# Optimization experiments

Hardware: AMD Instinct MI355X
Metric: run time of the kernel (lower is better)

Reference implementation:

```python
import jax, jax.numpy as jnp
import numpy as np

N, S, C, G = 50000, 16, 96, 6  # points, neighbours, embed_channels, groups
EPS = 1e-5


def bn(x, gamma, beta):
    # BatchNorm1d eval mode with default running stats (mean=0, var=1)
    return x * (gamma / jnp.sqrt(1.0 + EPS)) + beta


def setup_inputs() -> dict:
    key = jax.random.key(0)
    ks = jax.random.split(key, 16)
    d = {}
    d["feat"] = jax.random.normal(ks[0], (N, C), jnp.float32)
    d["coord"] = jax.random.uniform(ks[1], (N, 3), jnp.float32)
    d["reference_index"] = jax.random.randint(ks[2], (N, S), 0, N)

    def lin(k, fi, fo):
        return jax.random.normal(k, (fi, fo), jnp.float32) * 0.02

    # linear_q / linear_k / linear_v
    d["Wq"] = lin(ks[3], C, C); d["bq"] = jnp.zeros((C,), jnp.float32)
    d["gq"] = jnp.ones((C,), jnp.float32); d["betaq"] = jnp.zeros((C,), jnp.float32)
    d["Wk"] = lin(ks[4], C, C); d["bk"] = jnp.zeros((C,), jnp.float32)
    d["gk"] = jnp.ones((C,), jnp.float32); d["betak"] = jnp.zeros((C,), jnp.float32)
    d["Wv"] = lin(ks[5], C, C); d["bv"] = jnp.zeros((C,), jnp.float32)
    # linear_p_bias: Linear(3,C) -> BN -> ReLU -> Linear(C,C)
    d["Wp1"] = lin(ks[6], 3, C); d["bp1"] = jnp.zeros((C,), jnp.float32)
    d["gp"] = jnp.ones((C,), jnp.float32); d["betap"] = jnp.zeros((C,), jnp.float32)
    d["Wp2"] = lin(ks[7], C, C); d["bp2"] = jnp.zeros((C,), jnp.float32)
    # weight_encoding: Linear(C,G) -> BN(G) -> ReLU -> Linear(G,G)
    d["Ww1"] = lin(ks[8], C, G); d["bw1"] = jnp.zeros((G,), jnp.float32)
    d["gw"] = jnp.ones((G,), jnp.float32); d["betaw"] = jnp.zeros((G,), jnp.float32)
    d["Ww2"] = lin(ks[9], G, G); d["bw2"] = jnp.zeros((G,), jnp.float32)
    return d


def reference(feat, coord, Wq, bq, gq, betaq, Wk, bk, gk, betak, Wv, bv,
              Wp1, bp1, gp, betap, Wp2, bp2, Ww1, bw1, gw, betaw, Ww2, bw2,
              reference_index):
    q = jax.nn.relu(bn(feat @ Wq + bq, gq, betaq))          # [N, C]
    k = jax.nn.relu(bn(feat @ Wk + bk, gk, betak))          # [N, C]
    v = feat @ Wv + bv                                       # [N, C]

    # pointops.grouping: gather neighbours, with_xyz gives relative positions
    kg = k[reference_index]                                  # [N, S, C]
    vg = v[reference_index]                                  # [N, S, C]
    pos = coord[reference_index] - coord[:, None, :]         # [N, S, 3]

    relation_qk = kg - q[:, None, :]                         # [N, S, C]
    peb = jax.nn.relu(bn(pos @ Wp1 + bp1, gp, betap)) @ Wp2 + bp2  # [N, S, C]
    relation_qk = relation_qk + peb
    vg = vg + peb

    w = jax.nn.relu(bn(relation_qk @ Ww1 + bw1, gw, betaw)) @ Ww2 + bw2  # [N, S, G]
    w = jax.nn.softmax(w, axis=1)                            # softmax over neighbours
    mask = jnp.sign(reference_index + 1).astype(w.dtype)     # [N, S]
    w = w * mask[..., None]

    vg = vg.reshape(N, S, G, C // G)                         # [N, S, G, i]
    out = jnp.einsum('nsgi,nsg->ngi', vg, w).reshape(N, C)   # [N, C]
    return out
```

## Files before the change

### kernel.cpp

```cpp
#include <hip/hip_runtime.h>

typedef unsigned short u16;
typedef __attribute__((ext_vector_type(8))) short short8;
typedef __attribute__((ext_vector_type(4))) float f32x4;

__device__ __forceinline__ u16 f2bf(float f) {
    unsigned int x = __float_as_uint(f);
    unsigned int r = x + 0x7fffu + ((x >> 16) & 1u);
    return (u16)(r >> 16);
}
__device__ __forceinline__ unsigned int pk2(float lo, float hi) {
    return ((unsigned int)f2bf(hi) << 16) | (unsigned int)f2bf(lo);
}
__device__ __forceinline__ float2 bf2x(unsigned int d) {
    float2 r;
    r.x = __uint_as_float(d << 16);
    r.y = __uint_as_float(d & 0xffff0000u);
    return r;
}
__device__ __forceinline__ void bf8x(uint4 v, float* o) {
    float2 a = bf2x(v.x); o[0] = a.x; o[1] = a.y;
    float2 b = bf2x(v.y); o[2] = b.x; o[3] = b.y;
    float2 c = bf2x(v.z); o[4] = c.x; o[5] = c.y;
    float2 d = bf2x(v.w); o[6] = d.x; o[7] = d.y;
}
__device__ __forceinline__ float rfl_f(float x) {
    return __uint_as_float(__builtin_amdgcn_readfirstlane(__float_as_uint(x)));
}

#define CC 96
#define SS 16
#define GG 6
#define BN_INV 0.99999500003749969f
#define ABLK 768
#define TOTW (ABLK * 4)

#define WB_ODD 2496
#define WB_WPW 4992
#define WB_TOT 5304

__global__ __launch_bounds__(256) void prep_kernel(
    const float* __restrict__ Wq, const float* __restrict__ Wk, const float* __restrict__ Wv,
    const float* __restrict__ Wp2, const float* __restrict__ Ww1,
    const float* __restrict__ bp2, const float* __restrict__ bw1,
    u16* __restrict__ WcatT, unsigned int* __restrict__ gWB, float* __restrict__ cvec)
{
    int t = blockIdx.x * 256 + threadIdx.x;
    if (t < 13824) {
        int c = t / 48, j2 = t % 48;
        const float* src = (c < 96) ? Wq : (c < 192) ? Wk : Wv;
        int cc = c % 96;
        float a = src[(2 * j2) * CC + cc];
        float b = src[(2 * j2 + 1) * CC + cc];
        ((unsigned int*)WcatT)[t] = pk2(a, b);
    } else if (t < 13824 + WB_TOT) {
        int i = t - 13824;
        if (i < WB_WPW) {
            int arr = i / WB_ODD;
            int r = i % WB_ODD;
            int c2 = r / 52, rr = r % 52;
            unsigned int d = 0;
            if (rr < 48) {
                int c = 2 * c2 + arr;
                d = pk2(Wp2[(2 * rr) * CC + c], Wp2[(2 * rr + 1) * CC + c]);
            }
            gWB[i] = d;
        } else {
            int r = i - WB_WPW;
            int g = r / 52, rr = r % 52;
            unsigned int d = 0;
            if (rr < 48) {
                float a = 0.f, b = 0.f;
                for (int c = 0; c < CC; ++c) {
                    float wg = Ww1[c * GG + g];
                    a = fmaf(Wp2[(2 * rr) * CC + c], wg, a);
                    b = fmaf(Wp2[(2 * rr + 1) * CC + c], wg, b);
                }
                d = pk2(a, b);
            }
            gWB[i] = d;
        }
    } else if (t < 13824 + WB_TOT + GG) {
        int g = t - (13824 + WB_TOT);
        float acc = bw1[g];
        for (int c = 0; c < CC; ++c)
            acc = fmaf(bp2[c], Ww1[c * GG + g], acc);
        cvec[g] = acc;
    }
}

__global__ __launch_bounds__(256) void fcvt_kernel(
    const float* __restrict__ feat, u16* __restrict__ featB, int total4)
{
    int i = blockIdx.x * 256 + threadIdx.x;
    if (i < total4) {
        float4 v = *(const float4*)(feat + (size_t)i * 4);
        ushort4 o;
        o.x = f2bf(v.x); o.y = f2bf(v.y); o.z = f2bf(v.z); o.w = f2bf(v.w);
        *(ushort4*)(featB + (size_t)i * 4) = o;
    }
}

#define SBS 104
__global__ __launch_bounds__(256, 2) void gemm_qkv(
    const u16* __restrict__ featB, const u16* __restrict__ WcatT,
    const float* __restrict__ bq, const float* __restrict__ gq, const float* __restrict__ betaq,
    const float* __restrict__ bk, const float* __restrict__ gk, const float* __restrict__ betak,
    const float* __restrict__ bv, const float* __restrict__ Ww1,
    u16* __restrict__ v_bf, float* __restrict__ KW1, float* __restrict__ qW1, int N)
{
    __shared__ u16 sB[288 * SBS];
    const int t = threadIdx.x;

    for (int i = t; i < 288 * 12; i += 256) {
        int row = i / 12, c8 = i % 12;
        *(float4*)(sB + row * SBS + c8 * 8) = *(const float4*)(WcatT + row * CC + c8 * 8);
    }
    __syncthreads();

    const int wave = t >> 6, lane = t & 63;
    const int m = lane & 15, quad = lane >> 4;
    const int rowbase = blockIdx.x * 64 + wave * 16;

    int arow = rowbase + m;
    if (arow >= N) arow = 0;

    short8 a[3];
    #pragma unroll
    for (int kk = 0; kk < 3; ++kk)
        a[kk] = *(const short8*)(featB + (size_t)arow * CC + kk * 32 + quad * 8);

    f32x4 acc[18];
    #pragma unroll
    for (int nt = 0; nt < 18; ++nt) acc[nt] = (f32x4){0.f, 0.f, 0.f, 0.f};

    #pragma unroll
    for (int kk = 0; kk < 3; ++kk) {
        #pragma unroll
        for (int nt = 0; nt < 18; ++nt) {
            short8 b = *(const short8*)(sB + (nt * 16 + m) * SBS + kk * 32 + quad * 8);
            acc[nt] = __builtin_amdgcn_mfma_f32_16x16x32_bf16(a[kk], b, acc[nt], 0, 0, 0);
        }
    }

    int orow[4];
    #pragma unroll
    for (int i = 0; i < 4; ++i) orow[i] = rowbase + quad * 4 + i;
    const int cloc = m;

    #pragma unroll
    for (int nt6 = 0; nt6 < 6; ++nt6) {
        int c = nt6 * 16 + cloc;
        float bvv = bv[c];
        #pragma unroll
        for (int i = 0; i < 4; ++i)
            if (orow[i] < N)
                v_bf[(size_t)orow[i] * CC + c] = f2bf(acc[12 + nt6][i] + bvv);
    }

    #pragma unroll
    for (int mat = 0; mat < 2; ++mat) {
        const float* bb_ = mat ? bk : bq;
        const float* gg_ = mat ? gk : gq;
        const float* be_ = mat ? betak : betaq;
        float red[4][6];
        #pragma unroll
        for (int i = 0; i < 4; ++i)
            #pragma unroll
            for (int g = 0; g < 6; ++g) red[i][g] = 0.f;

        #pragma unroll
        for (int nt6 = 0; nt6 < 6; ++nt6) {
            int nt = mat * 6 + nt6;
            int c = nt6 * 16 + cloc;
            float bb = bb_[c], sc = gg_[c] * BN_INV, be = be_[c];
            float w1r[6];
            #pragma unroll
            for (int g = 0; g < 6; ++g) w1r[g] = Ww1[c * GG + g];
            #pragma unroll
            for (int i = 0; i < 4; ++i) {
                float act = fmaxf(0.f, fmaf(acc[nt][i] + bb, sc, be));
                #pragma unroll
                for (int g = 0; g < 6; ++g)
                    red[i][g] = fmaf(act, w1r[g], red[i][g]);
            }
        }
        #pragma unroll
        for (int st = 1; st < 16; st <<= 1)
            #pragma unroll
            for (int i = 0; i < 4; ++i)
                #pragma unroll
                for (int g = 0; g < 6; ++g)
                    red[i][g] += __shfl_xor(red[i][g], st);

        float* dst = mat ? KW1 : qW1;
        #pragma unroll
        for (int g = 0; g < 6; ++g)
            if (cloc == g)
                #pragma unroll
                for (int i = 0; i < 4; ++i)
                    if (orow[i] < N)
                        dst[(size_t)orow[i] * 8 + g] = red[i][g];
    }
}

__global__ __launch_bounds__(256) void attn_kernel(
    const float* __restrict__ coord, const int* __restrict__ ref,
    const float* __restrict__ Wp1, const float* __restrict__ bp1, const float* __restrict__ gp, const float* __restrict__ betap,
    const float* __restrict__ bp2,
    const float* __restrict__ gw, const float* __restrict__ betaw,
    const float* __restrict__ Ww2, const float* __restrict__ bw2,
    const u16* __restrict__ v_bf, const float* __restrict__ KW1, const float* __restrict__ qW1,
    const unsigned int* __restrict__ gWB, const float* __restrict__ cvec,
    float* __restrict__ out, int N)
{
    __shared__ __align__(16) unsigned int sWB[WB_TOT];
    __shared__ __align__(16) unsigned int shh[4][832];
    __shared__ __align__(16) uint4 swt[4][SS];
    __shared__ __align__(16) float sHs[4][600];
    __shared__ __align__(16) float4 sposx[4][SS];
    __shared__ int sidxx[4][SS];

    const int t = threadIdx.x;
    for (int i = t; i < WB_TOT; i += 256) sWB[i] = gWB[i];
    __syncthreads();

    const int w = t >> 6, lane = t & 63;
    const int wid = blockIdx.x * 4 + w;
    unsigned int* shw = shh[w];
    uint4* swtw = swt[w];
    float* sHsw = sHs[w];
    float4* sposw = sposx[w];
    int* sidxw = sidxx[w];

    const int  L = (lane < 48) ? lane : 47;
    const bool actv = lane < 48;
    const int  cA = 2 * L;
    const int  gL = L >> 3;
    const int  s16 = lane & 15, qq = lane >> 4;

    const float spA = gp[cA] * BN_INV, spB = gp[cA + 1] * BN_INV;
    const float w1xA = Wp1[cA] * spA, w1yA = Wp1[CC + cA] * spA, w1zA = Wp1[2 * CC + cA] * spA;
    const float w1xB = Wp1[cA + 1] * spB, w1yB = Wp1[CC + cA + 1] * spB, w1zB = Wp1[2 * CC + cA + 1] * spB;
    const float b1A = fmaf(bp1[cA], spA, betap[cA]);
    const float b1B = fmaf(bp1[cA + 1], spB, betap[cA + 1]);
    const float bpA = bp2[cA], bpB = bp2[cA + 1];

    int idxreg = 0;
    if (lane < SS && wid < N) idxreg = ref[wid * SS + s16];

    for (int n = wid; n < N; n += TOTW) {
        if (lane < SS) sidxw[s16] = idxreg;
        float4 kAv = {0,0,0,0}; float2 kBv = {0,0};
        if (lane < SS) {
            int j = idxreg;
            float4 P;
            P.x = coord[j * 3 + 0] - coord[n * 3 + 0];
            P.y = coord[j * 3 + 1] - coord[n * 3 + 1];
            P.z = coord[j * 3 + 2] - coord[n * 3 + 2];
            P.w = 0.f;
            sposw[s16] = P;
            const float* kr = KW1 + (size_t)idxreg * 8;
            kAv = *(const float4*)kr; kBv = *(const float2*)(kr + 4);
        }
        float qc[GG];
        {
            int nu = __builtin_amdgcn_readfirstlane(n);
            const float* qr = qW1 + (size_t)nu * 8;
            #pragma unroll
            for (int g = 0; g < GG; ++g)
                qc[g] = rfl_f(cvec[g] - qr[g]);
        }
        {
            int nn = n + TOTW;
            if (lane < SS && nn < N) idxreg = ref[nn * SS + s16];
        }

        if (actv) {
            #pragma unroll
            for (int s = 0; s < SS; ++s) {
                float4 P = sposw[s];
                float hA = fmaxf(0.f, fmaf(P.x, w1xA, fmaf(P.y, w1yA, fmaf(P.z, w1zA, b1A))));
                float hB = fmaxf(0.f, fmaf(P.x, w1xB, fmaf(P.y, w1yB, fmaf(P.z, w1zB, b1B))));
                shw[s * 52 + L] = pk2(hA, hB);
            }
        }

        float acc[GG];
        {
            const unsigned int* hrow = shw + 52 * s16 + 12 * qq;
            const unsigned int* wbase = sWB + WB_WPW + 12 * qq;
            #pragma unroll
            for (int g = 0; g < GG; ++g) acc[g] = 0.f;
            #pragma unroll
            for (int c3 = 0; c3 < 3; ++c3) {
                float hg[8];
                bf8x(*(const uint4*)(hrow + 4 * c3), hg);
                #pragma unroll
                for (int g = 0; g < GG; ++g) {
                    float wg[8];
                    bf8x(*(const uint4*)(wbase + g * 52 + 4 * c3), wg);
                    float a = acc[g];
                    #pragma unroll
                    for (int u = 0; u < 8; ++u)
                        a = fmaf(hg[u], wg[u], a);
                    acc[g] = a;
                }
            }
            #pragma unroll
            for (int g = 0; g < GG; ++g) {
                acc[g] += __shfl_xor(acc[g], 16);
                acc[g] += __shfl_xor(acc[g], 32);
            }
        }

        unsigned int vpre[SS];
        #pragma unroll
        for (int s = 0; s < SS; ++s) {
            int jj = sidxw[s];
            vpre[s] = *(const unsigned int*)(v_bf + (size_t)jj * CC + cA);
        }

        if (lane < SS) {
            float tv[GG];
            tv[0] = acc[0] + kAv.x + qc[0];
            tv[1] = acc[1] + kAv.y + qc[1];
            tv[2] = acc[2] + kAv.z + qc[2];
            tv[3] = acc[3] + kAv.w + qc[3];
            tv[4] = acc[4] + kBv.x + qc[4];
            tv[5] = acc[5] + kBv.y + qc[5];
            float a6[GG];
            #pragma unroll
            for (int g = 0; g < GG; ++g)
                a6[g] = fmaxf(0.f, fmaf(tv[g], gw[g] * BN_INV, betaw[g]));
            float e[GG];
            #pragma unroll
            for (int gg2 = 0; gg2 < GG; ++gg2) {
                float lv = bw2[gg2];
                #pragma unroll
                for (int g2 = 0; g2 < GG; ++g2)
                    lv = fmaf(a6[g2], Ww2[g2 * GG + gg2], lv);
                e[gg2] = __expf(lv);
            }
            float wgt[GG];
            #pragma unroll
            for (int g = 0; g < GG; ++g) {
                float ssum = e[g];
                ssum += __shfl_xor(ssum, 1);
                ssum += __shfl_xor(ssum, 2);
                ssum += __shfl_xor(ssum, 4);
                ssum += __shfl_xor(ssum, 8);
                wgt[g] = e[g] / ssum;
            }
            uint4 wt;
            wt.x = pk2(wgt[0], wgt[1]);
            wt.y = pk2(wgt[2], wgt[3]);
            wt.z = pk2(wgt[4], wgt[5]);
            wt.w = 0u;
            swtw[s16] = wt;
        }

        float accA = bpA, accB = bpB;
        {
            float hsA[GG] = {0.f,0.f,0.f,0.f,0.f,0.f};
            float hsB[GG] = {0.f,0.f,0.f,0.f,0.f,0.f};
            #pragma unroll
            for (int s = 0; s < SS; ++s) {
                uint4 wt = swtw[s];
                float2 w01 = bf2x(wt.x), w23 = bf2x(wt.y), w45 = bf2x(wt.z);
                float2 h2 = bf2x(shw[s * 52 + L]);
                hsA[0] = fmaf(w01.x, h2.x, hsA[0]); hsB[0] = fmaf(w01.x, h2.y, hsB[0]);
                hsA[1] = fmaf(w01.y, h2.x, hsA[1]); hsB[1] = fmaf(w01.y, h2.y, hsB[1]);
                hsA[2] = fmaf(w23.x, h2.x, hsA[2]); hsB[2] = fmaf(w23.x, h2.y, hsB[2]);
                hsA[3] = fmaf(w23.y, h2.x, hsA[3]); hsB[3] = fmaf(w23.y, h2.y, hsB[3]);
                hsA[4] = fmaf(w45.x, h2.x, hsA[4]); hsB[4] = fmaf(w45.x, h2.y, hsB[4]);
                hsA[5] = fmaf(w45.y, h2.x, hsA[5]); hsB[5] = fmaf(w45.y, h2.y, hsB[5]);
                float wsel = (gL < 2) ? (gL == 0 ? w01.x : w01.y)
                           : (gL < 4) ? (gL == 2 ? w23.x : w23.y)
                                      : (gL == 4 ? w45.x : w45.y);
                float2 v2 = bf2x(vpre[s]);
                accA = fmaf(v2.x, wsel, accA);
                accB = fmaf(v2.y, wsel, accB);
            }
            if (actv) {
                #pragma unroll
                for (int g = 0; g < GG; ++g)
                    *(float2*)(sHsw + g * 100 + cA) = make_float2(hsA[g], hsB[g]);
            }
        }

        if (actv) {
            const float* hrg = sHsw + gL * 100;
            const unsigned int* wrE = sWB + L * 52;
            const unsigned int* wrO = sWB + WB_ODD + L * 52;
            #pragma unroll
            for (int u = 0; u < 12; ++u) {
                float4 hb0 = *(const float4*)(hrg + 8 * u);
                float4 hb1 = *(const float4*)(hrg + 8 * u + 4);
                float we[8], wo[8];
                bf8x(*(const uint4*)(wrE + 4 * u), we);
                bf8x(*(const uint4*)(wrO + 4 * u), wo);
                accA = fmaf(hb0.x, we[0], accA); accB = fmaf(hb0.x, wo[0], accB);
                accA = fmaf(hb0.y, we[1], accA); accB = fmaf(hb0.y, wo[1], accB);
                accA = fmaf(hb0.z, we[2], accA); accB = fmaf(hb0.z, wo[2], accB);
                accA = fmaf(hb0.w, we[3], accA); accB = fmaf(hb0.w, wo[3], accB);
                accA = fmaf(hb1.x, we[4], accA); accB = fmaf(hb1.x, wo[4], accB);
                accA = fmaf(hb1.y, we[5], accA); accB = fmaf(hb1.y, wo[5], accB);
                accA = fmaf(hb1.z, we[6], accA); accB = fmaf(hb1.z, wo[6], accB);
                accA = fmaf(hb1.w, we[7], accA); accB = fmaf(hb1.w, wo[7], accB);
            }
            *(float2*)(out + (size_t)n * CC + cA) = make_float2(accA, accB);
        }
    }
}

extern "C" void kernel_launch(void* const* d_in, const int* in_sizes, int n_in,
                              void* d_out, int out_size, void* d_ws, size_t ws_size,
                              hipStream_t stream) {
    const float* feat  = (const float*)d_in[0];
    const float* coord = (const float*)d_in[1];
    const int*   ref   = (const int*)d_in[2];
    const float* Wq = (const float*)d_in[3],  *bq = (const float*)d_in[4],  *gq = (const float*)d_in[5],  *betaq = (const float*)d_in[6];
    const float* Wk = (const float*)d_in[7],  *bk = (const float*)d_in[8],  *gk = (const float*)d_in[9],  *betak = (const float*)d_in[10];
    const float* Wv = (const float*)d_in[11], *bv = (const float*)d_in[12];
    const float* Wp1 = (const float*)d_in[13], *bp1 = (const float*)d_in[14], *gp = (const float*)d_in[15], *betap = (const float*)d_in[16];
    const float* Wp2 = (const float*)d_in[17], *bp2 = (const float*)d_in[18];
    const float* Ww1 = (const float*)d_in[19], *bw1 = (const float*)d_in[20], *gw = (const float*)d_in[21], *betaw = (const float*)d_in[22];
    const float* Ww2 = (const float*)d_in[23], *bw2 = (const float*)d_in[24];

    const int N = in_sizes[0] / CC;

    float* wsf = (float*)d_ws;
    float* KW1 = wsf;
    float* qW1 = KW1 + (size_t)N * 8;
    float* cvec = qW1 + (size_t)N * 8;
    unsigned int* gWB = (unsigned int*)(cvec + 32);
    u16* WcatT = (u16*)(gWB + 5312);
    u16* featB = WcatT + 288 * CC;
    u16* v_bf = featB + (size_t)N * CC;

    const int prep_total = 13824 + WB_TOT + GG;
    prep_kernel<<<dim3((prep_total + 255) / 256), dim3(256), 0, stream>>>(
        Wq, Wk, Wv, Wp2, Ww1, bp2, bw1, WcatT, gWB, cvec);

    const int total4 = N * CC / 4;
    fcvt_kernel<<<dim3((total4 + 255) / 256), dim3(256), 0, stream>>>(feat, featB, total4);

    gemm_qkv<<<dim3((N + 63) / 64), dim3(256), 0, stream>>>(
        featB, WcatT, bq, gq, betaq, bk, gk, betak, bv, Ww1,
        v_bf, KW1, qW1, N);

    attn_kernel<<<dim3(ABLK), dim3(256), 0, stream>>>(
        coord, ref, Wp1, bp1, gp, betap, bp2, gw, betaw, Ww2, bw2,
        v_bf, KW1, qW1, gWB, cvec, (float*)d_out, N);
}
```

Baseline: 424.7 us.

## Rebalance shared-memory precision in attn kernel and cap VGPRs

The per-neighbour hidden position activations now stay in fp32 in shared memory (stride 100) instead of packed bf16, which removes pack and unpack work in two consumer loops. The softmax weights and the grouped hidden sums use packed fp16 via the cvt_pkrtz instruction instead of bf16, which halves the sHs buffer and its LDS reads in the final 96-wide projection. An amdgpu_num_vgpr(168) attribute caps register use to control occupancy. The trade-off is more LDS for the hidden buffer, possible fp16 range and precision effects from round-toward-zero packing, and possible spills if the VGPR cap is tight.

```diff
diff --git a/kernel.cpp b/kernel.cpp
--- a/kernel.cpp
+++ b/kernel.cpp
@@ -3,6 +3,7 @@
 typedef unsigned short u16;
 typedef __attribute__((ext_vector_type(8))) short short8;
 typedef __attribute__((ext_vector_type(4))) float f32x4;
+typedef __attribute__((ext_vector_type(2))) __fp16 h16x2;
 
 __device__ __forceinline__ u16 f2bf(float f) {
     unsigned int x = __float_as_uint(f);
@@ -23,6 +24,20 @@
     float2 b = bf2x(v.y); o[2] = b.x; o[3] = b.y;
     float2 c = bf2x(v.z); o[4] = c.x; o[5] = c.y;
     float2 d = bf2x(v.w); o[6] = d.x; o[7] = d.y;
+}
+__device__ __forceinline__ unsigned int pkh2(float lo, float hi) {
+    h16x2 h = __builtin_amdgcn_cvt_pkrtz(lo, hi);
+    return __builtin_bit_cast(unsigned int, h);
+}
+__device__ __forceinline__ float2 h2x(unsigned int d) {
+    h16x2 h = __builtin_bit_cast(h16x2, d);
+    return make_float2((float)h.x, (float)h.y);
+}
+__device__ __forceinline__ void h8x(uint4 v, float* o) {
+    float2 a = h2x(v.x); o[0] = a.x; o[1] = a.y;
+    float2 b = h2x(v.y); o[2] = b.x; o[3] = b.y;
+    float2 c = h2x(v.z); o[4] = c.x; o[5] = c.y;
+    float2 d = h2x(v.w); o[6] = d.x; o[7] = d.y;
 }
 __device__ __forceinline__ float rfl_f(float x) {
     return __uint_as_float(__builtin_amdgcn_readfirstlane(__float_as_uint(x)));
@@ -204,7 +219,7 @@
     }
 }
 
-__global__ __launch_bounds__(256) void attn_kernel(
+__global__ __launch_bounds__(256) __attribute__((amdgpu_num_vgpr(168))) void attn_kernel(
     const float* __restrict__ coord, const int* __restrict__ ref,
     const float* __restrict__ Wp1, const float* __restrict__ bp1, const float* __restrict__ gp, const float* __restrict__ betap,
     const float* __restrict__ bp2,
@@ -215,9 +230,9 @@
     float* __restrict__ out, int N)
 {
     __shared__ __align__(16) unsigned int sWB[WB_TOT];
-    __shared__ __align__(16) unsigned int shh[4][832];
+    __shared__ __align__(16) float shh[4][SS * 100];
     __shared__ __align__(16) uint4 swt[4][SS];
-    __shared__ __align__(16) float sHs[4][600];
+    __shared__ __align__(16) unsigned int sHsH[4][312];
     __shared__ __align__(16) float4 sposx[4][SS];
     __shared__ int sidxx[4][SS];
 
@@ -227,9 +242,9 @@
 
     const int w = t >> 6, lane = t & 63;
     const int wid = blockIdx.x * 4 + w;
-    unsigned int* shw = shh[w];
+    float* shw = shh[w];
     uint4* swtw = swt[w];
-    float* sHsw = sHs[w];
+    unsigned int* sHsw = sHsH[w];
     float4* sposw = sposx[w];
     int* sidxw = sidxx[w];
 
@@ -282,28 +297,29 @@
                 float4 P = sposw[s];
                 float hA = fmaxf(0.f, fmaf(P.x, w1xA, fmaf(P.y, w1yA, fmaf(P.z, w1zA, b1A))));
                 float hB = fmaxf(0.f, fmaf(P.x, w1xB, fmaf(P.y, w1yB, fmaf(P.z, w1zB, b1B))));
-                shw[s * 52 + L] = pk2(hA, hB);
+                *(float2*)(shw + s * 100 + cA) = make_float2(hA, hB);
             }
         }
 
         float acc[GG];
         {
-            const unsigned int* hrow = shw + 52 * s16 + 12 * qq;
+            const float* hrow = shw + 100 * s16 + 24 * qq;
             const unsigned int* wbase = sWB + WB_WPW + 12 * qq;
             #pragma unroll
             for (int g = 0; g < GG; ++g) acc[g] = 0.f;
             #pragma unroll
             for (int c3 = 0; c3 < 3; ++c3) {
-                float hg[8];
-                bf8x(*(const uint4*)(hrow + 4 * c3), hg);
+                float4 h0 = *(const float4*)(hrow + 8 * c3);
+                float4 h1 = *(const float4*)(hrow + 8 * c3 + 4);
                 #pragma unroll
                 for (int g = 0; g < GG; ++g) {
                     float wg[8];
                     bf8x(*(const uint4*)(wbase + g * 52 + 4 * c3), wg);
                     float a = acc[g];
-                    #pragma unroll
-                    for (int u = 0; u < 8; ++u)
-                        a = fmaf(hg[u], wg[u], a);
+                    a = fmaf(h0.x, wg[0], a); a = fmaf(h0.y, wg[1], a);
+                    a = fmaf(h0.z, wg[2], a); a = fmaf(h0.w, wg[3], a);
+                    a = fmaf(h1.x, wg[4], a); a = fmaf(h1.y, wg[5], a);
+                    a = fmaf(h1.z, wg[6], a); a = fmaf(h1.w, wg[7], a);
                     acc[g] = a;
                 }
             }
@@ -353,9 +369,9 @@
                 wgt[g] = e[g] / ssum;
             }
             uint4 wt;
-            wt.x = pk2(wgt[0], wgt[1]);
-            wt.y = pk2(wgt[2], wgt[3]);
-            wt.z = pk2(wgt[4], wgt[5]);
+            wt.x = pkh2(wgt[0], wgt[1]);
+            wt.y = pkh2(wgt[2], wgt[3]);
+            wt.z = pkh2(wgt[4], wgt[5]);
             wt.w = 0u;
             swtw[s16] = wt;
         }
@@ -367,8 +383,8 @@
             #pragma unroll
             for (int s = 0; s < SS; ++s) {
                 uint4 wt = swtw[s];
-                float2 w01 = bf2x(wt.x), w23 = bf2x(wt.y), w45 = bf2x(wt.z);
-                float2 h2 = bf2x(shw[s * 52 + L]);
+                float2 w01 = h2x(wt.x), w23 = h2x(wt.y), w45 = h2x(wt.z);
+                float2 h2 = *(const float2*)(shw + s * 100 + cA);
                 hsA[0] = fmaf(w01.x, h2.x, hsA[0]); hsB[0] = fmaf(w01.x, h2.y, hsB[0]);
                 hsA[1] = fmaf(w01.y, h2.x, hsA[1]); hsB[1] = fmaf(w01.y, h2.y, hsB[1]);
                 hsA[2] = fmaf(w23.x, h2.x, hsA[2]); hsB[2] = fmaf(w23.x, h2.y, hsB[2]);
@@ -385,29 +401,28 @@
             if (actv) {
                 #pragma unroll
                 for (int g = 0; g < GG; ++g)
-                    *(float2*)(sHsw + g * 100 + cA) = make_float2(hsA[g], hsB[g]);
+                    sHsw[g * 52 + L] = pkh2(hsA[g], hsB[g]);
             }
         }
 
         if (actv) {
-            const float* hrg = sHsw + gL * 100;
+            const unsigned int* hrg = sHsw + gL * 52;
             const unsigned int* wrE = sWB + L * 52;
             const unsigned int* wrO = sWB + WB_ODD + L * 52;
             #pragma unroll
             for (int u = 0; u < 12; ++u) {
-                float4 hb0 = *(const float4*)(hrg + 8 * u);
-                float4 hb1 = *(const float4*)(hrg + 8 * u + 4);
-                float we[8], wo[8];
+                float hb[8], we[8], wo[8];
+                h8x(*(const uint4*)(hrg + 4 * u), hb);
                 bf8x(*(const uint4*)(wrE + 4 * u), we);
                 bf8x(*(const uint4*)(wrO + 4 * u), wo);
-                accA = fmaf(hb0.x, we[0], accA); accB = fmaf(hb0.x, wo[0], accB);
-                accA = fmaf(hb0.y, we[1], accA); accB = fmaf(hb0.y, wo[1], accB);
-                accA = fmaf(hb0.z, we[2], accA); accB = fmaf(hb0.z, wo[2], accB);
-                accA = fmaf(hb0.w, we[3], accA); accB = fmaf(hb0.w, wo[3], accB);
-                accA = fmaf(hb1.x, we[4], accA); accB = fmaf(hb1.x, wo[4], accB);
-                accA = fmaf(hb1.y, we[5], accA); accB = fmaf(hb1.y, wo[5], accB);
-                accA = fmaf(hb1.z, we[6], accA); accB = fmaf(hb1.z, wo[6], accB);
-                accA = fmaf(hb1.w, we[7], accA); accB = fmaf(hb1.w, wo[7], accB);
+                accA = fmaf(hb[0], we[0], accA); accB = fmaf(hb[0], wo[0], accB);
+                accA = fmaf(hb[1], we[1], accA); accB = fmaf(hb[1], wo[1], accB);
+                accA = fmaf(hb[2], we[2], accA); accB = fmaf(hb[2], wo[2], accB);
+                accA = fmaf(hb[3], we[3], accA); accB = fmaf(hb[3], wo[3], accB);
+                accA = fmaf(hb[4], we[4], accA); accB = fmaf(hb[4], wo[4], accB);
+                accA = fmaf(hb[5], we[5], accA); accB = fmaf(hb[5], wo[5], accB);
+                accA = fmaf(hb[6], we[6], accA); accB = fmaf(hb[6], wo[6], accB);
+                accA = fmaf(hb[7], we[7], accA); accB = fmaf(hb[7], wo[7], accB);
             }
             *(float2*)(out + (size_t)n * CC + cA) = make_float2(accA, accB);
         }
```

After: 480.2 us. 1.13x slower.
